# Optimization experiments

Measured on AMD Instinct MI355X. Metric: run time of the kernel, lower is better.

Reference implementation:

```python
import jax, jax.numpy as jnp
import numpy as np
from jax import lax

B, C, H, W = 8, 256, 64, 64
A = 9                      # anchors per location (3 scales x 3 ratios)
STRIDE = 16
IMG = 1024                 # image_size
POST_NMS = 1000            # post_nms_top_n (also used as pre-NMS slice, as in source)
NMS_THR = 0.7
BBOX_XFORM_CLIP = 4.135166556742356  # log(1000/16)


def make_anchors():
    # ordering must match torch reshape (B,4,-1): index = a*H*W + h*W + w
    scales = jnp.array([128.0, 256.0, 512.0], dtype=jnp.float32)
    ratios = jnp.array([0.5, 1.0, 2.0], dtype=jnp.float32)
    ws = (scales[:, None] / jnp.sqrt(ratios)[None, :]).reshape(-1)  # [A]
    hs = (scales[:, None] * jnp.sqrt(ratios)[None, :]).reshape(-1)  # [A]
    cx = (jnp.arange(W, dtype=jnp.float32) + 0.5) * STRIDE
    cy = (jnp.arange(H, dtype=jnp.float32) + 0.5) * STRIDE
    cx = jnp.broadcast_to(cx[None, None, :], (A, H, W))
    cy = jnp.broadcast_to(cy[None, :, None], (A, H, W))
    aw = jnp.broadcast_to(ws[:, None, None], (A, H, W))
    ah = jnp.broadcast_to(hs[:, None, None], (A, H, W))
    anchors = jnp.stack([cx - aw / 2, cy - ah / 2, cx + aw / 2, cy + ah / 2], axis=-1)
    return anchors.reshape(-1, 4)  # [K,4] xyxy


def conv2d(x, w, b, pad):
    y = lax.conv_general_dilated(x, w, (1, 1), [(pad, pad), (pad, pad)],
                                 dimension_numbers=("NCHW", "OIHW", "NCHW"))
    return y + b[None, :, None, None]


def decode(t, anchors):
    # t: [K,4] (tx,ty,tw,th); anchors: [K,4] xyxy -> boxes xyxy
    aw = anchors[:, 2] - anchors[:, 0]
    ah = anchors[:, 3] - anchors[:, 1]
    acx = anchors[:, 0] + 0.5 * aw
    acy = anchors[:, 1] + 0.5 * ah
    cx = t[:, 0] * aw + acx
    cy = t[:, 1] * ah + acy
    w = jnp.exp(jnp.clip(t[:, 2], -BBOX_XFORM_CLIP, BBOX_XFORM_CLIP)) * aw
    h = jnp.exp(jnp.clip(t[:, 3], -BBOX_XFORM_CLIP, BBOX_XFORM_CLIP)) * ah
    return jnp.stack([cx - 0.5 * w, cy - 0.5 * h, cx + 0.5 * w, cy + 0.5 * h], axis=-1)


def box_iou(a, b):
    area_a = (a[:, 2] - a[:, 0]) * (a[:, 3] - a[:, 1])
    area_b = (b[:, 2] - b[:, 0]) * (b[:, 3] - b[:, 1])
    lt = jnp.maximum(a[:, None, :2], b[None, :, :2])
    rb = jnp.minimum(a[:, None, 2:], b[None, :, 2:])
    wh = jnp.clip(rb - lt, 0.0)
    inter = wh[..., 0] * wh[..., 1]
    return inter / (area_a[:, None] + area_b[None, :] - inter)


def filter_one(boxes, scores):
    # boxes [K,4], scores [K]. Faithful to source: torch.sort ascending,
    # slice to POST_NMS, then class-agnostic greedy NMS, pad to POST_NMS.
    order = jnp.argsort(lax.stop_gradient(scores))        # ascending (torch.sort default)
    idx = order[:POST_NMS]
    b = boxes[idx]
    s = scores[idx]
    # batched_nms internally processes boxes in descending-score order
    o2 = jnp.argsort(-lax.stop_gradient(s))
    b2 = b[o2]
    s2 = s[o2]
    iou = box_iou(b2, b2)  # [POST_NMS, POST_NMS]
    N = POST_NMS
    pos = jnp.arange(N)

    def body(i, keep):
        sup = (iou[i] > NMS_THR) & (pos > i) & keep[i]
        return keep & ~sup

    keep = lax.fori_loop(0, N, body, jnp.ones((N,), dtype=bool))
    # pack kept boxes (descending-score order) to the front, zero-pad the rest
    perm = jnp.argsort(jnp.where(keep, pos, N + pos))
    valid = pos < jnp.sum(keep)
    out_b = jnp.where(valid[:, None], b2[perm], 0.0)
    out_s = jnp.where(valid, s2[perm], 0.0)
    return out_b, out_s


def setup_inputs() -> dict:
    key = jax.random.key(0)
    ks = jax.random.split(key, 5)
    x = jax.random.normal(ks[0], (B, C, H, W), dtype=jnp.float32)
    conv_w = jax.random.normal(ks[1], (C, C, 3, 3), dtype=jnp.float32) * 0.01
    conv_b = jnp.zeros((C,), dtype=jnp.float32)
    box_w = jax.random.normal(ks[2], (4 * A, C, 1, 1), dtype=jnp.float32) * 0.01
    box_b = jnp.zeros((4 * A,), dtype=jnp.float32)
    obj_w = jax.random.normal(ks[3], (A, C, 1, 1), dtype=jnp.float32) * 0.01
    obj_b = jnp.zeros((A,), dtype=jnp.float32)
    return {"x": x, "conv_w": conv_w, "conv_b": conv_b,
            "box_w": box_w, "box_b": box_b, "obj_w": obj_w, "obj_b": obj_b}


def reference(x, conv_w, conv_b, box_w, box_b, obj_w, obj_b):
    feats = jax.nn.relu(conv2d(x, conv_w, conv_b, 1))        # [B,C,H,W]
    t = conv2d(feats, box_w, box_b, 0)                        # [B,4A,H,W]
    o = conv2d(feats, obj_w, obj_b, 0)                        # [B,A,H,W]
    t = t.reshape(B, 4, -1).transpose(0, 2, 1)                # [B,K,4]
    obj = o.reshape(B, -1)                                    # [B,K]
    anchors = make_anchors()                                  # [K,4]
    props = jax.vmap(lambda ti: decode(ti, anchors))(t)       # [B,K,4]
    props = jnp.clip(props, 0.0, float(IMG))                  # clip_boxes_to_image
    out_b, out_s = jax.vmap(filter_one)(props, obj)           # [B,POST_NMS,4],[B,POST_NMS]
    return jnp.concatenate([out_b, out_s[..., None]], axis=-1)  # [B,POST_NMS,5]
```

## Files before the change

### kernel.cpp

```cpp
#include <hip/hip_runtime.h>

#define B_ 8
#define C_ 256
#define H_ 64
#define W_ 64
#define HW_ 4096
#define HP_ 66
#define HWP_ 4224
#define A_ 9
#define SITES 36864
#define NPOST 1000
#define XCLIPF 4.1351666f
#define IMGF 1024.0f

__device__ inline unsigned keyf(float v) {
  unsigned u = __float_as_uint(v);
  return (u & 0x80000000u) ? ~u : (u | 0x80000000u);
}

__device__ __forceinline__ float dpp_shr1(float v) {
  return __int_as_float(__builtin_amdgcn_update_dpp(
      0, __float_as_int(v), 0x111 , 0xf, 0xf, true));
}
__device__ __forceinline__ float dpp_shl1(float v) {
  return __int_as_float(__builtin_amdgcn_update_dpp(
      0, __float_as_int(v), 0x101 , 0xf, 0xf, true));
}

__global__ __launch_bounds__(256) void prep(
    const float* __restrict__ x, const float* __restrict__ w,
    const float* __restrict__ box_w, const float* __restrict__ obj_w,
    float* __restrict__ xp, float* __restrict__ wq, float* __restrict__ wt) {
  int blk = blockIdx.x;
  if (blk < 8448) {
    int t = blk * 256 + threadIdx.x;
    int c4 = t & 15;
    int rr = (t >> 4) % HP_;
    int bc = t / (HP_ * 16);
    float4 v = make_float4(0.f, 0.f, 0.f, 0.f);
    if (rr >= 1 && rr <= 64)
      v = ((const float4*)x)[(size_t)bc * (HW_ / 4) + (size_t)(rr - 1) * 16 + c4];
    ((float4*)xp)[(size_t)bc * (HWP_ / 4) + (size_t)rr * 16 + c4] = v;
  } else if (blk < 8448 + 2304) {
    int idx = (blk - 8448) * 256 + threadIdx.x;
    int quad = idx / (256 * 36);
    int rem  = idx % (256 * 36);
    int ci = rem / 36;
    int k  = rem % 36;
    int q = k / 9, t = k % 9;
    wq[idx] = w[((size_t)(quad * 4 + q)) * (C_ * 9) + (size_t)ci * 9 + t];
  } else {
    int idx = (blk - 8448 - 2304) * 256 + threadIdx.x;
    if (idx < C_ * 45) {
      int ci = idx / 45, jj = idx % 45;
      wt[idx] = (jj < 36) ? box_w[(size_t)jj * C_ + ci]
                          : obj_w[(size_t)(jj - 36) * C_ + ci];
    }
  }
}

__global__ __launch_bounds__(256, 2) void conv3_4co(
    const float* __restrict__ xp, const float* __restrict__ wq,
    const float* __restrict__ bias, float* __restrict__ feats) {
#pragma clang fp contract(off)
  int b       = blockIdx.x & 7;
  int j       = blockIdx.x >> 3;
  int quad    = j & 63;
  int quarter = j >> 6;
  int co0 = quad << 2;
  int row16 = threadIdx.x >> 4;
  int chunk = threadIdx.x & 15;
  int gr = (quarter << 4) + row16;
  int c0 = chunk << 2;

  const float* px0 = xp + (size_t)b * C_ * HWP_ + (size_t)gr * W_ + c0;
  const float* wqb = wq + (size_t)quad * (C_ * 36);

  float acc[4][4][9];
#pragma unroll
  for (int q = 0; q < 4; ++q)
#pragma unroll
    for (int p = 0; p < 4; ++p)
#pragma unroll
      for (int t = 0; t < 9; ++t) acc[q][p][t] = 0.f;

#pragma unroll 2
  for (int ci = 0; ci < C_; ++ci) {
    const float* pr = px0 + (size_t)ci * HWP_;
    float4 tA = ((const float4*)(pr      ))[0];
    float4 mA = ((const float4*)(pr +  64))[0];
    float4 bA = ((const float4*)(pr + 128))[0];

    float T[6], M[6], Bo[6];
    T[1]=tA.x;  T[2]=tA.y;  T[3]=tA.z;  T[4]=tA.w;
    M[1]=mA.x;  M[2]=mA.y;  M[3]=mA.z;  M[4]=mA.w;
    Bo[1]=bA.x; Bo[2]=bA.y; Bo[3]=bA.z; Bo[4]=bA.w;

    T[0]  = dpp_shr1(T[4]);   T[5]  = dpp_shl1(T[1]);
    M[0]  = dpp_shr1(M[4]);   M[5]  = dpp_shl1(M[1]);
    Bo[0] = dpp_shr1(Bo[4]);  Bo[5] = dpp_shl1(Bo[1]);

    const float* wrow = wqb + ci * 36;
    float w9[4][9];
#pragma unroll
    for (int q = 0; q < 4; ++q)
#pragma unroll
      for (int t = 0; t < 9; ++t) w9[q][t] = wrow[q * 9 + t];

#pragma unroll
    for (int q = 0; q < 4; ++q)
#pragma unroll
      for (int p = 0; p < 4; ++p) {
        acc[q][p][0] = fmaf(w9[q][0], T[p],     acc[q][p][0]);
        acc[q][p][1] = fmaf(w9[q][1], T[p+1],   acc[q][p][1]);
        acc[q][p][2] = fmaf(w9[q][2], T[p+2],   acc[q][p][2]);
        acc[q][p][3] = fmaf(w9[q][3], M[p],     acc[q][p][3]);
        acc[q][p][4] = fmaf(w9[q][4], M[p+1],   acc[q][p][4]);
        acc[q][p][5] = fmaf(w9[q][5], M[p+2],   acc[q][p][5]);
        acc[q][p][6] = fmaf(w9[q][6], Bo[p],    acc[q][p][6]);
        acc[q][p][7] = fmaf(w9[q][7], Bo[p+1],  acc[q][p][7]);
        acc[q][p][8] = fmaf(w9[q][8], Bo[p+2],  acc[q][p][8]);
      }
  }

#pragma unroll
  for (int q = 0; q < 4; ++q) {
    float bv = bias[co0 + q];
    float ov[4];
#pragma unroll
    for (int p = 0; p < 4; ++p) {
      float a = 0.f;
#pragma unroll
      for (int t = 0; t < 9; ++t) a = a + acc[q][p][t];
      a = a + bv;
      ov[p] = a > 0.f ? a : 0.f;
    }
    float4* fo = (float4*)(feats + ((size_t)b * C_ + co0 + q) * HW_ + (size_t)gr * W_ + c0);
    fo[0] = make_float4(ov[0], ov[1], ov[2], ov[3]);
  }
}

__global__ __launch_bounds__(64) void conv1_all45(
    const float* __restrict__ feats, const float* __restrict__ wt,
    const float* __restrict__ box_b, const float* __restrict__ obj_b,
    float* __restrict__ tbox, float* __restrict__ scores) {
#pragma clang fp contract(off)
  int gidx = blockIdx.x * 64 + threadIdx.x;
  int b  = gidx >> 12;
  int hw = gidx & 4095;
  const float* f = feats + (size_t)b * C_ * HW_ + hw;
  float acc[45];
#pragma unroll
  for (int jj = 0; jj < 45; ++jj) acc[jj] = 0.f;
#pragma unroll 4
  for (int ci = 0; ci < C_; ++ci) {
    float fv = f[(size_t)ci * HW_];
    const float* wr = wt + ci * 45;
#pragma unroll
    for (int jj = 0; jj < 45; ++jj)
      acc[jj] = fmaf(wr[jj], fv, acc[jj]);
  }
#pragma unroll
  for (int c = 0; c < 36; ++c) {
    int k = c / 9, a = c - k * 9;
    tbox[(size_t)b * 4 * SITES + (size_t)k * SITES + (size_t)a * HW_ + hw] = acc[c] + box_b[c];
  }
#pragma unroll
  for (int a = 0; a < 9; ++a)
    scores[(size_t)b * SITES + (size_t)a * HW_ + hw] = acc[36 + a] + obj_b[a];
}

__global__ __launch_bounds__(1024) void select_sort_decode(
    const float* __restrict__ scores, const float* __restrict__ tbox,
    float* __restrict__ s2, float* __restrict__ b2) {
#pragma clang fp contract(off)
  int b = blockIdx.x;
  const float* s = scores + (size_t)b * SITES;
  __shared__ unsigned hist[256];
  __shared__ unsigned sh_prefix, sh_mask, sh_cless;
  __shared__ int sh_target;
  __shared__ int sh_cnt, sh_eq;
  __shared__ int sh_sel[1024];
  __shared__ int sh_eqList[4096];
  __shared__ float ss[NPOST];
  __shared__ int st[NPOST];
  if (threadIdx.x == 0) {
    sh_prefix = 0; sh_mask = 0; sh_target = NPOST - 1; sh_cless = 0;
    sh_cnt = 0; sh_eq = 0;
  }
  for (int shift = 24; shift >= 0; shift -= 8) {
    if (threadIdx.x < 256) hist[threadIdx.x] = 0;
    __syncthreads();
    unsigned prefix = sh_prefix, mask = sh_mask;
    for (int i = threadIdx.x; i < SITES; i += 1024) {
      unsigned k = keyf(s[i]);
      if ((k & mask) == prefix) atomicAdd(&hist[(k >> shift) & 255u], 1u);
    }
    __syncthreads();
    if (threadIdx.x == 0) {
      unsigned cum = 0; int t = sh_target; int v = 0;
      for (; v < 256; ++v) {
        unsigned h = hist[v];
        if (cum + h > (unsigned)t) break;
        cum += h;
      }
      sh_prefix |= ((unsigned)v) << shift;
      sh_mask   |= 0xFFu << shift;
      sh_target  = t - (int)cum;
      sh_cless  += cum;
    }
    __syncthreads();
  }
  unsigned K = sh_prefix;
  int need = NPOST - (int)sh_cless;
  for (int i = threadIdx.x; i < SITES; i += 1024) {
    unsigned k = keyf(s[i]);
    if (k < K) {
      int pos = atomicAdd(&sh_cnt, 1);
      sh_sel[pos] = i;
    } else if (k == K) {
      int e = atomicAdd(&sh_eq, 1);
      if (e < 4096) sh_eqList[e] = i;
    }
  }
  __syncthreads();
  {
    int E = sh_eq; if (E > 4096) E = 4096;
    int base = sh_cnt;
    for (int t = threadIdx.x; t < E; t += 1024) {
      int site = sh_eqList[t];
      int rank = 0;
      for (int q = 0; q < E; ++q) rank += (sh_eqList[q] < site);
      if (rank < need) sh_sel[base + rank] = site;
    }
  }
  __syncthreads();
  for (int t = threadIdx.x; t < NPOST; t += 1024) {
    int site = sh_sel[t];
    st[t] = site;
    ss[t] = s[site];
  }
  __syncthreads();
  if (threadIdx.x < NPOST) {
    int r = threadIdx.x;
    float sr = ss[r]; int sir = st[r];
    int d = 0;
    for (int q = 0; q < NPOST; ++q) {
      float sq = ss[q];
      d += (int)((sq > sr) || (sq == sr && st[q] < sir));
    }
    s2[(size_t)b * NPOST + d] = sr;
    int site = sir;
    int a = site / HW_;
    int hw = site - a * HW_;
    int h = hw / W_, wc = hw - h * W_;
    int sidx = a / 3, ridx = a - sidx * 3;
    float scale = (sidx == 0) ? 128.f : ((sidx == 1) ? 256.f : 512.f);
    float ratio = (ridx == 0) ? 0.5f : ((ridx == 1) ? 1.0f : 2.0f);
    float sq = sqrtf(ratio);
    float wsa = scale / sq;
    float hsa = scale * sq;
    float cx = ((float)wc + 0.5f) * 16.f;
    float cy = ((float)h + 0.5f) * 16.f;
    float ax1 = cx - wsa * 0.5f;
    float ay1 = cy - hsa * 0.5f;
    float ax2 = cx + wsa * 0.5f;
    float ay2 = cy + hsa * 0.5f;
    float aw = ax2 - ax1, ah = ay2 - ay1;
    float m1 = 0.5f * aw, m2 = 0.5f * ah;
    float acx = ax1 + m1, acy = ay1 + m2;
    const float* tb = tbox + (size_t)b * 4 * SITES + site;
    float t0 = tb[0];
    float t1 = tb[SITES];
    float t2 = tb[2 * (size_t)SITES];
    float t3 = tb[3 * (size_t)SITES];
    if (t2 < -XCLIPF) t2 = -XCLIPF;
    if (t2 > XCLIPF) t2 = XCLIPF;
    if (t3 < -XCLIPF) t3 = -XCLIPF;
    if (t3 > XCLIPF) t3 = XCLIPF;
    float pm0 = t0 * aw;  float pcx = pm0 + acx;
    float pm1 = t1 * ah;  float pcy = pm1 + acy;
    float pw = expf(t2) * aw;
    float ph = expf(t3) * ah;
    float hw0 = 0.5f * pw, hh0 = 0.5f * ph;
    float x1 = pcx - hw0, y1 = pcy - hh0;
    float x2 = pcx + hw0, y2 = pcy + hh0;
    x1 = x1 < 0.f ? 0.f : (x1 > IMGF ? IMGF : x1);
    y1 = y1 < 0.f ? 0.f : (y1 > IMGF ? IMGF : y1);
    x2 = x2 < 0.f ? 0.f : (x2 > IMGF ? IMGF : x2);
    y2 = y2 < 0.f ? 0.f : (y2 > IMGF ? IMGF : y2);
    float* o = b2 + ((size_t)b * NPOST + d) * 4;
    o[0] = x1; o[1] = y1; o[2] = x2; o[3] = y2;
  }
}

__global__ __launch_bounds__(256) void mask_kernel(
    const float* __restrict__ b2, unsigned long long* __restrict__ sup) {
#pragma clang fp contract(off)
  int b = blockIdx.x / 63;
  int i0 = (blockIdx.x % 63) * 16;
  __shared__ float bs[NPOST * 4];
  __shared__ float area[NPOST];
  for (int t = threadIdx.x; t < NPOST * 4; t += 256) bs[t] = b2[(size_t)b * NPOST * 4 + t];
  __syncthreads();
  for (int t = threadIdx.x; t < NPOST; t += 256)
    area[t] = (bs[t * 4 + 2] - bs[t * 4]) * (bs[t * 4 + 3] - bs[t * 4 + 1]);
  __syncthreads();
  int i = i0 + (threadIdx.x & 15);
  int wd = threadIdx.x >> 4;
  if (i >= NPOST) return;
  float ax1 = bs[i * 4], ay1 = bs[i * 4 + 1], ax2 = bs[i * 4 + 2], ay2 = bs[i * 4 + 3];
  float aa = area[i];
  unsigned long long m = 0;
  for (int bit = 0; bit < 64; ++bit) {
    int j = wd * 64 + bit;
    if (j > i && j < NPOST) {
      float lx = fmaxf(ax1, bs[j * 4]);
      float ly = fmaxf(ay1, bs[j * 4 + 1]);
      float rx = fminf(ax2, bs[j * 4 + 2]);
      float ry = fminf(ay2, bs[j * 4 + 3]);
      float iw = rx - lx; if (iw < 0.f) iw = 0.f;
      float ih = ry - ly; if (ih < 0.f) ih = 0.f;
      float inter = iw * ih;
      float denom = (aa + area[j]) - inter;
      float iou = inter / denom;
      if (iou > 0.7f) m |= 1ull << bit;
    }
  }
  sup[((size_t)b * NPOST + i) * 16 + wd] = m;
}

__global__ __launch_bounds__(64) void nms_out(
    const unsigned long long* __restrict__ sup, const float* __restrict__ b2,
    const float* __restrict__ s2, float* __restrict__ out) {
  int b = blockIdx.x;
  int lane = threadIdx.x;
  unsigned long long kw = 0;
  if (lane < 16) kw = (lane < 15) ? ~0ull : ((1ull << 40) - 1);
  const unsigned long long* ms = sup + (size_t)b * NPOST * 16;
  unsigned long long mb[8];
#pragma unroll
  for (int k = 0; k < 8; ++k)
    mb[k] = (lane < 16) ? ms[(size_t)k * 16 + lane] : 0ull;
  for (int i0 = 0; i0 < NPOST; i0 += 8) {
    unsigned long long nb[8];
#pragma unroll
    for (int k = 0; k < 8; ++k) {
      int nx = i0 + 8 + k;
      nb[k] = (nx < NPOST && lane < 16) ? ms[(size_t)nx * 16 + lane] : 0ull;
    }
#pragma unroll
    for (int k = 0; k < 8; ++k) {
      int i = i0 + k;
      unsigned long long w = __shfl(kw, i >> 6, 64);
      if ((w >> (i & 63)) & 1ull) {
        if (lane < 16) kw &= ~mb[k];
      }
    }
#pragma unroll
    for (int k = 0; k < 8; ++k) mb[k] = nb[k];
  }
  __shared__ unsigned long long keeps[16];
  if (lane < 16) keeps[lane] = kw;
  __syncthreads();
  int total = 0;
#pragma unroll
  for (int k = 0; k < 16; ++k) total += __popcll(keeps[k]);
  for (int i = lane; i < NPOST; i += 64) {
    int w = i >> 6;
    int before = 0;
    for (int k = 0; k < w; ++k) before += __popcll(keeps[k]);
    before += __popcll(keeps[w] & ((1ull << (i & 63)) - 1));
    bool kept = (keeps[w] >> (i & 63)) & 1ull;
    if (kept) {
      size_t ob = (size_t)b * (NPOST * 5) + (size_t)before * 5;
      const float* src = b2 + ((size_t)b * NPOST + i) * 4;
      out[ob + 0] = src[0];
      out[ob + 1] = src[1];
      out[ob + 2] = src[2];
      out[ob + 3] = src[3];
      out[ob + 4] = s2[(size_t)b * NPOST + i];
    }
    if (i >= total) {
      size_t ob = (size_t)b * (NPOST * 5) + (size_t)i * 5;
      for (int c = 0; c < 5; ++c) out[ob + c] = 0.f;
    }
  }
}

extern "C" void kernel_launch(void* const* d_in, const int* in_sizes, int n_in,
                              void* d_out, int out_size, void* d_ws, size_t ws_size,
                              hipStream_t stream) {
  const float *x = nullptr, *conv_w = nullptr, *conv_b = nullptr,
              *box_w = nullptr, *box_b = nullptr, *obj_w = nullptr, *obj_b = nullptr;
  for (int i = 0; i < n_in; ++i) {
    switch (in_sizes[i]) {
      case 8388608: x = (const float*)d_in[i]; break;
      case 589824:  conv_w = (const float*)d_in[i]; break;
      case 256:     conv_b = (const float*)d_in[i]; break;
      case 9216:    box_w = (const float*)d_in[i]; break;
      case 36:      box_b = (const float*)d_in[i]; break;
      case 2304:    obj_w = (const float*)d_in[i]; break;
      case 9:       obj_b = (const float*)d_in[i]; break;
    }
  }
  float* out = (float*)d_out;

  char* p = (char*)d_ws;
  auto alloc = [&](size_t n) { char* q = p; p += (n + 255) & ~255ull; return (void*)q; };
  float* feats  = (float*)alloc((size_t)B_ * C_ * HW_ * 4);
  float* tbox   = (float*)alloc((size_t)B_ * 4 * SITES * 4);
  float* scores = (float*)alloc((size_t)B_ * SITES * 4);
  float* xpad   = (float*)alloc((size_t)B_ * C_ * HWP_ * 4);
  float* wq     = (float*)alloc((size_t)64 * C_ * 36 * 4);
  float* wt     = (float*)alloc((size_t)C_ * 45 * 4);
  float* s2     = (float*)alloc((size_t)B_ * NPOST * 4);
  float* b2     = (float*)alloc((size_t)B_ * NPOST * 4 * 4);
  unsigned long long* sup = (unsigned long long*)alloc((size_t)B_ * NPOST * 16 * 8);

  hipLaunchKernelGGL(prep, dim3(8448 + 2304 + 45), dim3(256), 0, stream,
                     x, conv_w, box_w, obj_w, xpad, wq, wt);
  hipLaunchKernelGGL(conv3_4co, dim3(B_ * 64 * 4), dim3(256), 0, stream,
                     xpad, wq, conv_b, feats);
  hipLaunchKernelGGL(conv1_all45, dim3(B_ * HW_ / 64), dim3(64), 0, stream,
                     feats, wt, box_b, obj_b, tbox, scores);
  hipLaunchKernelGGL(select_sort_decode, dim3(B_), dim3(1024), 0, stream,
                     scores, tbox, s2, b2);
  hipLaunchKernelGGL(mask_kernel, dim3(B_ * 63), dim3(256), 0, stream, b2, sup);
  hipLaunchKernelGGL(nms_out, dim3(B_), dim3(64), 0, stream, sup, b2, s2, out);
}
```

Before: 869.1 us.

## Split 1x1 head conv into 5 channel groups; warp-aggregate selection atomics

The 1x1 head conv now splits its 45 output channels into five groups of 9 across more threads, each using fewer accumulator registers. Each thread now reads the feature vector five times instead of once, but occupancy and parallelism rise. In the top-k radix select, histogram increments and compaction appends are aggregated per wavefront with ballot, shuffle and popcount, cutting shared-memory atomic contention. The order within sh_sel and the equal-key list may change, but ranks are recomputed afterwards.

```diff
diff --git a/kernel.cpp b/kernel.cpp
--- a/kernel.cpp
+++ b/kernel.cpp
@@ -140,34 +140,39 @@
   }
 }
 
-__global__ __launch_bounds__(64) void conv1_all45(
+__global__ __launch_bounds__(256) void conv1_split5(
     const float* __restrict__ feats, const float* __restrict__ wt,
     const float* __restrict__ box_b, const float* __restrict__ obj_b,
     float* __restrict__ tbox, float* __restrict__ scores) {
 #pragma clang fp contract(off)
-  int gidx = blockIdx.x * 64 + threadIdx.x;
-  int b  = gidx >> 12;
-  int hw = gidx & 4095;
+  int b = blockIdx.x & 7;
+  int j = blockIdx.x >> 3;
+  int gidx2 = j * 256 + threadIdx.x;
+  int grp = gidx2 >> 12;
+  int hw  = gidx2 & 4095;
+  int cbase = grp * 9;
   const float* f = feats + (size_t)b * C_ * HW_ + hw;
-  float acc[45];
-#pragma unroll
-  for (int jj = 0; jj < 45; ++jj) acc[jj] = 0.f;
+  float acc[9];
+#pragma unroll
+  for (int jj = 0; jj < 9; ++jj) acc[jj] = 0.f;
 #pragma unroll 4
   for (int ci = 0; ci < C_; ++ci) {
     float fv = f[(size_t)ci * HW_];
-    const float* wr = wt + ci * 45;
-#pragma unroll
-    for (int jj = 0; jj < 45; ++jj)
+    const float* wr = wt + ci * 45 + cbase;
+#pragma unroll
+    for (int jj = 0; jj < 9; ++jj)
       acc[jj] = fmaf(wr[jj], fv, acc[jj]);
   }
-#pragma unroll
-  for (int c = 0; c < 36; ++c) {
-    int k = c / 9, a = c - k * 9;
-    tbox[(size_t)b * 4 * SITES + (size_t)k * SITES + (size_t)a * HW_ + hw] = acc[c] + box_b[c];
-  }
-#pragma unroll
-  for (int a = 0; a < 9; ++a)
-    scores[(size_t)b * SITES + (size_t)a * HW_ + hw] = acc[36 + a] + obj_b[a];
+  if (grp < 4) {
+#pragma unroll
+    for (int jj = 0; jj < 9; ++jj)
+      tbox[(size_t)b * 4 * SITES + (size_t)grp * SITES + (size_t)jj * HW_ + hw] =
+          acc[jj] + box_b[cbase + jj];
+  } else {
+#pragma unroll
+    for (int jj = 0; jj < 9; ++jj)
+      scores[(size_t)b * SITES + (size_t)jj * HW_ + hw] = acc[jj] + obj_b[jj];
+  }
 }
 
 __global__ __launch_bounds__(1024) void select_sort_decode(
@@ -184,6 +189,7 @@
   __shared__ int sh_eqList[4096];
   __shared__ float ss[NPOST];
   __shared__ int st[NPOST];
+  int lane = threadIdx.x & 63;
   if (threadIdx.x == 0) {
     sh_prefix = 0; sh_mask = 0; sh_target = NPOST - 1; sh_cless = 0;
     sh_cnt = 0; sh_eq = 0;
@@ -194,7 +200,16 @@
     unsigned prefix = sh_prefix, mask = sh_mask;
     for (int i = threadIdx.x; i < SITES; i += 1024) {
       unsigned k = keyf(s[i]);
-      if ((k & mask) == prefix) atomicAdd(&hist[(k >> shift) & 255u], 1u);
+      bool v = ((k & mask) == prefix);
+      unsigned bin = (k >> shift) & 255u;
+      unsigned long long remaining = __ballot(v);
+      while (remaining) {
+        int src = __ffsll((long long)remaining) - 1;
+        unsigned bsel = (unsigned)__shfl((int)bin, src, 64);
+        unsigned long long match = __ballot(v && (bin == bsel));
+        if (lane == src) atomicAdd(&hist[bsel], (unsigned)__popcll(match));
+        remaining &= ~match;
+      }
     }
     __syncthreads();
     if (threadIdx.x == 0) {
@@ -215,12 +230,28 @@
   int need = NPOST - (int)sh_cless;
   for (int i = threadIdx.x; i < SITES; i += 1024) {
     unsigned k = keyf(s[i]);
-    if (k < K) {
-      int pos = atomicAdd(&sh_cnt, 1);
-      sh_sel[pos] = i;
-    } else if (k == K) {
-      int e = atomicAdd(&sh_eq, 1);
-      if (e < 4096) sh_eqList[e] = i;
+    bool lt = (k < K), eq = (k == K);
+    unsigned long long mlt = __ballot(lt);
+    if (mlt) {
+      int leader = __ffsll((long long)mlt) - 1;
+      int base = 0;
+      if (lane == leader) base = atomicAdd(&sh_cnt, (int)__popcll(mlt));
+      base = __shfl(base, leader, 64);
+      if (lt) {
+        int off = (int)__popcll(mlt & ((1ull << lane) - 1ull));
+        sh_sel[base + off] = i;
+      }
+    }
+    unsigned long long meq = __ballot(eq);
+    if (meq) {
+      int leader = __ffsll((long long)meq) - 1;
+      int base = 0;
+      if (lane == leader) base = atomicAdd(&sh_eq, (int)__popcll(meq));
+      base = __shfl(base, leader, 64);
+      if (eq) {
+        int e = base + (int)__popcll(meq & ((1ull << lane) - 1ull));
+        if (e < 4096) sh_eqList[e] = i;
+      }
     }
   }
   __syncthreads();
@@ -422,7 +453,7 @@
                      x, conv_w, box_w, obj_w, xpad, wq, wt);
   hipLaunchKernelGGL(conv3_4co, dim3(B_ * 64 * 4), dim3(256), 0, stream,
                      xpad, wq, conv_b, feats);
-  hipLaunchKernelGGL(conv1_all45, dim3(B_ * HW_ / 64), dim3(64), 0, stream,
+  hipLaunchKernelGGL(conv1_split5, dim3(8 * 80), dim3(256), 0, stream,
                      feats, wt, box_b, obj_b, tbox, scores);
   hipLaunchKernelGGL(select_sort_decode, dim3(B_), dim3(1024), 0, stream,
                      scores, tbox, s2, b2);
```

After: 954.9 us. +9.9%, slower.
